# Kernel tuning notes

Measured on AMD Instinct MI355X. Metric: run time of the kernel, lower is better.

## Reference

```python
import jax, jax.numpy as jnp
import numpy as np

N_NODES = 50000
N_EDGES = 640000
HID = 128
EDGE_FEAT = 4
NUM_G = 20
R_MIN, R_MAX = 0.0, 10.0

def setup_inputs() -> dict:
    key = jax.random.key(0)
    ks = jax.random.split(key, 16)
    s = lambda d: 1.0 / np.sqrt(d)
    return {
        'h': jax.random.normal(ks[0], (N_NODES, HID), jnp.float32),
        'x': jax.random.normal(ks[1], (N_NODES, 3), jnp.float32),
        'edge_index': jax.random.randint(ks[2], (2, N_EDGES), 0, N_NODES, dtype=jnp.int64),
        'mask_ligand': jnp.ones((N_NODES,), jnp.float32),
        'edge_attr': jax.random.normal(ks[3], (N_EDGES, EDGE_FEAT), jnp.float32),
        'We1': jax.random.normal(ks[4], (2*HID+EDGE_FEAT+NUM_G, HID), jnp.float32) * s(2*HID+EDGE_FEAT+NUM_G),
        'be1': jnp.zeros((HID,), jnp.float32),
        'We2': jax.random.normal(ks[5], (HID, HID), jnp.float32) * s(HID),
        'be2': jnp.zeros((HID,), jnp.float32),
        'Winf': jax.random.normal(ks[6], (HID, 1), jnp.float32) * s(HID),
        'binf': jnp.zeros((1,), jnp.float32),
        'Wx1': jax.random.normal(ks[7], (HID, HID), jnp.float32) * s(HID),
        'bx1': jnp.zeros((HID,), jnp.float32),
        'Wx2': jax.random.normal(ks[8], (HID, 1), jnp.float32) * 0.001 * s(HID),
        'Wn1': jax.random.normal(ks[9], (2*HID, HID), jnp.float32) * s(2*HID),
        'bn1': jnp.zeros((HID,), jnp.float32),
        'Wn2': jax.random.normal(ks[10], (HID, HID), jnp.float32) * s(HID),
        'bn2': jnp.zeros((HID,), jnp.float32),
    }

def reference(h, x, edge_index, mask_ligand, edge_attr,
              We1, be1, We2, be2, Winf, binf, Wx1, bx1, Wx2, Wn1, bn1, Wn2, bn2):
    n = h.shape[0]
    src, dst = edge_index[0], edge_index[1]
    hi, hj = h[dst], h[src]                      # [E, H] gathers
    rel_x = x[dst] - x[src]                      # [E, 3]
    d_sq = jnp.sum(rel_x**2, axis=-1, keepdims=True)  # [E, 1]
    d = jnp.sqrt(d_sq + 1e-8)
    # GaussianSmearing(r_min=0, r_max=10, num_gaussians=20)
    offset = jnp.linspace(R_MIN, R_MAX, NUM_G, dtype=h.dtype)
    coeff = -0.5 / (offset[1] - offset[0])**2
    d_feat = jnp.exp(coeff * (d - offset)**2)    # [E, 20]
    edge_feat = jnp.concatenate([d_feat, edge_attr], axis=-1)
    # edge MLP (2 layers, silu, act_last=True)
    z = jnp.concatenate([hi, hj, edge_feat], axis=-1)
    mij = jax.nn.silu(jax.nn.silu(z @ We1 + be1) @ We2 + be2)  # [E, H]
    eij = jax.nn.sigmoid(mij @ Winf + binf)      # [E, 1]
    mi = jax.ops.segment_sum(mij * eij, dst, num_segments=n)   # [N, H]
    # node MLP (2 layers, silu, no act on last)
    nz = jnp.concatenate([mi, h], axis=-1)
    h_out = h + (jax.nn.silu(nz @ Wn1 + bn1) @ Wn2 + bn2)
    # coordinate update
    xg = jnp.tanh(jax.nn.silu(mij @ Wx1 + bx1) @ Wx2)          # [E, 1]
    delta_x = jax.ops.segment_sum(rel_x / (d + 1.0) * xg, dst, num_segments=n)
    x_out = x + delta_x * mask_ligand[:, None]
    return h_out, x_out
```

## Files before the change

kernel.cpp:

```cpp
#include <hip/hip_runtime.h>
#include <math.h>

#define NN 50000
#define NE 640000
#define H 128
#define EPB 32
#define NPB 32
#define ZB 296
#define BB 136
#define KP1 288
#define NZB 264

typedef __attribute__((ext_vector_type(8))) unsigned short u16x8;
typedef __attribute__((ext_vector_type(8))) __bf16 bf16x8;
typedef __attribute__((ext_vector_type(2))) __bf16 bf16x2;
typedef __attribute__((ext_vector_type(4))) float f32x4;

__device__ __forceinline__ float silu_f(float v) {
    return v / (1.0f + __expf(-v));
}

__device__ __forceinline__ unsigned short f2bf(float f) {
    unsigned int u = __builtin_bit_cast(unsigned int, f);
    u += 0x7FFFu + ((u >> 16) & 1u);
    return (unsigned short)(u >> 16);
}

__device__ __forceinline__ float bf2f(unsigned short s) {
    unsigned int u = ((unsigned int)s) << 16;
    return __builtin_bit_cast(float, u);
}

__device__ __forceinline__ unsigned int pkbf(float lo, float hi) {
#if __has_builtin(__builtin_amdgcn_cvt_pk_bf16_f32)
    bf16x2 v = __builtin_amdgcn_cvt_pk_bf16_f32(lo, hi);
    unsigned int r; __builtin_memcpy(&r, &v, 4); return r;
#else
    return (unsigned int)f2bf(lo) | ((unsigned int)f2bf(hi) << 16);
#endif
}

__device__ __forceinline__ f32x4 mfma16(u16x8 a, u16x8 b, f32x4 c) {
    return __builtin_amdgcn_mfma_f32_16x16x32_bf16(
        __builtin_bit_cast(bf16x8, a), __builtin_bit_cast(bf16x8, b), c, 0, 0, 0);
}

template<int KT, int INSTR, bool SYNC_BEFORE_EPI>
__device__ __forceinline__ void layer_mfma(
    const unsigned short* __restrict__ inbuf,
    const unsigned short* __restrict__ wt,
    const float* __restrict__ bias,
    unsigned short* __restrict__ outbuf,
    int wv, int quad, int r16)
{
    f32x4 acc[2][2] = {};
    const int F = wv * 32;
    #pragma unroll
    for (int ks = 0; ks < KT / 32; ks++) {
        int ko = ks * 32 + quad * 8;
        u16x8 b0 = *(const u16x8*)(inbuf + r16 * INSTR + ko);
        u16x8 b1 = *(const u16x8*)(inbuf + (16 + r16) * INSTR + ko);
        u16x8 a0 = *(const u16x8*)(wt + (size_t)(F + r16) * KT + ko);
        u16x8 a1 = *(const u16x8*)(wt + (size_t)(F + 16 + r16) * KT + ko);
        acc[0][0] = mfma16(a0, b0, acc[0][0]);
        acc[0][1] = mfma16(a0, b1, acc[0][1]);
        acc[1][0] = mfma16(a1, b0, acc[1][0]);
        acc[1][1] = mfma16(a1, b1, acc[1][1]);
    }
    if (SYNC_BEFORE_EPI) __syncthreads();
    #pragma unroll
    for (int rt = 0; rt < 2; rt++) {
        int f0 = F + rt * 16 + quad * 4;
        float4 bv = *(const float4*)(bias + f0);
        #pragma unroll
        for (int ci = 0; ci < 2; ci++) {
            int e = ci * 16 + r16;
            float s0 = silu_f(acc[rt][ci][0] + bv.x);
            float s1 = silu_f(acc[rt][ci][1] + bv.y);
            float s2 = silu_f(acc[rt][ci][2] + bv.z);
            float s3 = silu_f(acc[rt][ci][3] + bv.w);
            uint2 p = { pkbf(s0, s1), pkbf(s2, s3) };
            *(uint2*)(outbuf + e * BB + f0) = p;
        }
    }
}

__global__ __launch_bounds__(256) void convert_weights(
    const float* __restrict__ We1, const float* __restrict__ We2,
    const float* __restrict__ Wx1, const float* __restrict__ Wn1,
    const float* __restrict__ Wn2,
    unsigned short* __restrict__ w1t, unsigned short* __restrict__ w2t,
    unsigned short* __restrict__ wx1t, unsigned short* __restrict__ wn1t,
    unsigned short* __restrict__ wn2t)
{
    int i = blockIdx.x * 256 + threadIdx.x;
    const int S1 = 128 * KP1;
    const int S2 = 128 * 128;
    const int S3 = 128 * 256;
    if (i < S1) {
        int n = i / KP1, k = i % KP1;
        w1t[i] = (k < 280) ? f2bf(We1[k * H + n]) : (unsigned short)0;
    } else if (i < S1 + S2) {
        int j = i - S1; int n = j / H, k = j % H;
        w2t[j] = f2bf(We2[k * H + n]);
    } else if (i < S1 + 2 * S2) {
        int j = i - S1 - S2; int n = j / H, k = j % H;
        wx1t[j] = f2bf(Wx1[k * H + n]);
    } else if (i < S1 + 2 * S2 + S3) {
        int j = i - S1 - 2 * S2; int n = j / 256, k = j % 256;
        wn1t[j] = f2bf(Wn1[k * H + n]);
    } else if (i < S1 + 3 * S2 + S3) {
        int j = i - S1 - 2 * S2 - S3; int n = j / H, k = j % H;
        wn2t[j] = f2bf(Wn2[k * H + n]);
    }
}

__global__ __launch_bounds__(256) void zero_kernel(float4* __restrict__ p, int n4) {
    int i = blockIdx.x * 256 + threadIdx.x;
    if (i < n4) p[i] = make_float4(0.f, 0.f, 0.f, 0.f);
}

__global__ __launch_bounds__(256, 5) void edge_kernel(
    const float* __restrict__ h, const float* __restrict__ x,
    const int* __restrict__ ei, const float* __restrict__ edge_attr,
    const unsigned short* __restrict__ w1t, const float* __restrict__ be1,
    const unsigned short* __restrict__ w2t, const float* __restrict__ be2,
    const float* __restrict__ Winf, const float* __restrict__ binf,
    const unsigned short* __restrict__ wx1t, const float* __restrict__ bx1,
    const float* __restrict__ Wx2,
    float* __restrict__ mi, float* __restrict__ dx)
{
    __shared__ unsigned short zs[EPB * ZB];
    __shared__ unsigned short m2[EPB * BB];
    __shared__ float relx_s[EPB][3];
    __shared__ float eij_s[EPB];
    __shared__ float xg_s[EPB];
    __shared__ int dst_s[EPB];
    __shared__ int src_s[EPB];
    __shared__ float winf_s[H];
    __shared__ float wx2_s[H];

    unsigned short* m1 = zs;

    const int t = threadIdx.x;
    const int e0 = blockIdx.x * EPB;

    if (t < EPB) {
        src_s[t] = ei[e0 + t];
        dst_s[t] = ei[NE + e0 + t];
    }
    if (t >= 128 && t < 256) {
        winf_s[t - 128] = Winf[t - 128];
        wx2_s[t - 128] = Wx2[t - 128];
    }
    __syncthreads();

    {
        int e = t >> 3, l = t & 7;
        int s = src_s[e], d = dst_s[e];
        const float4* hd = (const float4*)(h + (size_t)d * H);
        const float4* hs = (const float4*)(h + (size_t)s * H);
        unsigned short* zr = zs + e * ZB;
        float4 v0 = hd[l * 4 + 0], v1 = hd[l * 4 + 1];
        float4 v2 = hd[l * 4 + 2], v3 = hd[l * 4 + 3];
        uint4 p0 = { pkbf(v0.x, v0.y), pkbf(v0.z, v0.w), pkbf(v1.x, v1.y), pkbf(v1.z, v1.w) };
        uint4 p1 = { pkbf(v2.x, v2.y), pkbf(v2.z, v2.w), pkbf(v3.x, v3.y), pkbf(v3.z, v3.w) };
        *(uint4*)(zr + l * 16) = p0;
        *(uint4*)(zr + l * 16 + 8) = p1;
        float4 w0 = hs[l * 4 + 0], w1 = hs[l * 4 + 1];
        float4 w2 = hs[l * 4 + 2], w3 = hs[l * 4 + 3];
        uint4 q0 = { pkbf(w0.x, w0.y), pkbf(w0.z, w0.w), pkbf(w1.x, w1.y), pkbf(w1.z, w1.w) };
        uint4 q1 = { pkbf(w2.x, w2.y), pkbf(w2.z, w2.w), pkbf(w3.x, w3.y), pkbf(w3.z, w3.w) };
        *(uint4*)(zr + 128 + l * 16) = q0;
        *(uint4*)(zr + 128 + l * 16 + 8) = q1;
    }
    if (t < EPB) {
        int s = src_s[t], d = dst_s[t];
        float rx = x[d * 3 + 0] - x[s * 3 + 0];
        float ry = x[d * 3 + 1] - x[s * 3 + 1];
        float rz = x[d * 3 + 2] - x[s * 3 + 2];
        float d2 = rx * rx + ry * ry + rz * rz;
        float dd = sqrtf(d2 + 1e-8f);
        float inv = 1.0f / (dd + 1.0f);
        relx_s[t][0] = rx * inv;
        relx_s[t][1] = ry * inv;
        relx_s[t][2] = rz * inv;
        const float step = 10.0f / 19.0f;
        const float coeff = -0.5f / (step * step);
        unsigned short* zr = zs + t * ZB;
        #pragma unroll
        for (int g = 0; g < 20; g++) {
            float df = dd - step * (float)g;
            zr[256 + g] = f2bf(__expf(coeff * df * df));
        }
        #pragma unroll
        for (int j = 0; j < 4; j++)
            zr[276 + j] = f2bf(edge_attr[(size_t)(e0 + t) * 4 + j]);
        #pragma unroll
        for (int j = 280; j < ZB; j++) zr[j] = 0;
    }
    __syncthreads();

    const int wv = t >> 6, lane = t & 63;
    const int quad = lane >> 4, r16 = lane & 15;

    layer_mfma<KP1, ZB, true>(zs, w1t, be1, m1, wv, quad, r16);
    __syncthreads();

    layer_mfma<H, BB, false>(m1, w2t, be2, m2, wv, quad, r16);
    __syncthreads();

    {
        int e = t >> 3, l = t & 7;
        const unsigned short* row = m2 + e * BB + l * 16;
        u16x8 v0 = *(const u16x8*)(row);
        u16x8 v1 = *(const u16x8*)(row + 8);
        float s = 0.0f;
        #pragma unroll
        for (int j = 0; j < 8; j++) {
            s += bf2f(v0[j]) * winf_s[l * 16 + j];
            s += bf2f(v1[j]) * winf_s[l * 16 + 8 + j];
        }
        s += __shfl_down(s, 4, 8);
        s += __shfl_down(s, 2, 8);
        s += __shfl_down(s, 1, 8);
        if (l == 0) eij_s[e] = 1.0f / (1.0f + __expf(-(s + binf[0])));
    }

    layer_mfma<H, BB, false>(m2, wx1t, bx1, m1, wv, quad, r16);
    __syncthreads();

    {
        int e = t >> 3, l = t & 7;
        const unsigned short* row = m1 + e * BB + l * 16;
        u16x8 v0 = *(const u16x8*)(row);
        u16x8 v1 = *(const u16x8*)(row + 8);
        float s = 0.0f;
        #pragma unroll
        for (int j = 0; j < 8; j++) {
            s += bf2f(v0[j]) * wx2_s[l * 16 + j];
            s += bf2f(v1[j]) * wx2_s[l * 16 + 8 + j];
        }
        s += __shfl_down(s, 4, 8);
        s += __shfl_down(s, 2, 8);
        s += __shfl_down(s, 1, 8);
        if (l == 0) xg_s[e] = tanhf(s);
    }
    __syncthreads();

    {
        int k = t & 127, eh = t >> 7;
        for (int e = eh; e < EPB; e += 2) {
            float mv = bf2f(m2[e * BB + k]) * eij_s[e];
            atomicAdd(&mi[(size_t)dst_s[e] * H + k], mv);
        }
        if (t < EPB * 3) {
            int e = t / 3, dim = t % 3;
            atomicAdd(&dx[(size_t)dst_s[e] * 3 + dim], relx_s[e][dim] * xg_s[e]);
        }
    }
}

__global__ __launch_bounds__(256, 6) void node_kernel(
    const float* __restrict__ h, const float* __restrict__ x,
    const float* __restrict__ mask,
    const unsigned short* __restrict__ wn1t, const float* __restrict__ bn1,
    const unsigned short* __restrict__ wn2t, const float* __restrict__ bn2,
    float* __restrict__ mi_hout, float* __restrict__ dx_xout)
{
    __shared__ unsigned short nzs[NPB * NZB];
    __shared__ unsigned short nbuf[NPB * BB];

    const int t = threadIdx.x;
    const int n0 = blockIdx.x * NPB;

    {
        int r = t >> 3, l = t & 7;
        int n = n0 + r;
        unsigned short* zr = nzs + r * NZB;
        if (n < NN) {
            const float4* mi4 = (const float4*)(mi_hout + (size_t)n * H);
            const float4* h4  = (const float4*)(h + (size_t)n * H);
            float4 v0 = mi4[l * 4 + 0], v1 = mi4[l * 4 + 1];
            float4 v2 = mi4[l * 4 + 2], v3 = mi4[l * 4 + 3];
            uint4 p0 = { pkbf(v0.x, v0.y), pkbf(v0.z, v0.w), pkbf(v1.x, v1.y), pkbf(v1.z, v1.w) };
            uint4 p1 = { pkbf(v2.x, v2.y), pkbf(v2.z, v2.w), pkbf(v3.x, v3.y), pkbf(v3.z, v3.w) };
            *(uint4*)(zr + l * 16) = p0;
            *(uint4*)(zr + l * 16 + 8) = p1;
            float4 w0 = h4[l * 4 + 0], w1 = h4[l * 4 + 1];
            float4 w2 = h4[l * 4 + 2], w3 = h4[l * 4 + 3];
            uint4 q0 = { pkbf(w0.x, w0.y), pkbf(w0.z, w0.w), pkbf(w1.x, w1.y), pkbf(w1.z, w1.w) };
            uint4 q1 = { pkbf(w2.x, w2.y), pkbf(w2.z, w2.w), pkbf(w3.x, w3.y), pkbf(w3.z, w3.w) };
            *(uint4*)(zr + 128 + l * 16) = q0;
            *(uint4*)(zr + 128 + l * 16 + 8) = q1;
        } else {
            uint4 zf = {0u, 0u, 0u, 0u};
            *(uint4*)(zr + l * 16) = zf;
            *(uint4*)(zr + l * 16 + 8) = zf;
            *(uint4*)(zr + 128 + l * 16) = zf;
            *(uint4*)(zr + 128 + l * 16 + 8) = zf;
        }
    }

    float xo = 0.f;
    int xn = -1, xdim = 0;
    if (t < NPB * 3) {
        int r = t / 3; xdim = t % 3;
        int n = n0 + r;
        if (n < NN) {
            xn = n;
            xo = x[(size_t)n * 3 + xdim] + dx_xout[(size_t)n * 3 + xdim] * mask[n];
        }
    }
    __syncthreads();

    if (xn >= 0) dx_xout[(size_t)xn * 3 + xdim] = xo;

    const int wv = t >> 6, lane = t & 63;
    const int quad = lane >> 4, r16 = lane & 15;

    layer_mfma<2 * H, NZB, false>(nzs, wn1t, bn1, nbuf, wv, quad, r16);
    __syncthreads();

    {
        f32x4 acc[2][2] = {};
        const int F = wv * 32;
        #pragma unroll
        for (int ks = 0; ks < H / 32; ks++) {
            int ko = ks * 32 + quad * 8;
            u16x8 b0 = *(const u16x8*)(nbuf + r16 * BB + ko);
            u16x8 b1 = *(const u16x8*)(nbuf + (16 + r16) * BB + ko);
            u16x8 a0 = *(const u16x8*)(wn2t + (size_t)(F + r16) * H + ko);
            u16x8 a1 = *(const u16x8*)(wn2t + (size_t)(F + 16 + r16) * H + ko);
            acc[0][0] = mfma16(a0, b0, acc[0][0]);
            acc[0][1] = mfma16(a0, b1, acc[0][1]);
            acc[1][0] = mfma16(a1, b0, acc[1][0]);
            acc[1][1] = mfma16(a1, b1, acc[1][1]);
        }
        #pragma unroll
        for (int rt = 0; rt < 2; rt++) {
            int f0 = F + rt * 16 + quad * 4;
            float4 bv = *(const float4*)(bn2 + f0);
            #pragma unroll
            for (int ci = 0; ci < 2; ci++) {
                int n = n0 + ci * 16 + r16;
                if (n < NN) {
                    float4 hv = *(const float4*)(h + (size_t)n * H + f0);
                    float4 o;
                    o.x = hv.x + acc[rt][ci][0] + bv.x;
                    o.y = hv.y + acc[rt][ci][1] + bv.y;
                    o.z = hv.z + acc[rt][ci][2] + bv.z;
                    o.w = hv.w + acc[rt][ci][3] + bv.w;
                    *(float4*)(mi_hout + (size_t)n * H + f0) = o;
                }
            }
        }
    }
}

extern "C" void kernel_launch(void* const* d_in, const int* in_sizes, int n_in,
                              void* d_out, int out_size, void* d_ws, size_t ws_size,
                              hipStream_t stream) {
    const float* h     = (const float*)d_in[0];
    const float* x     = (const float*)d_in[1];
    const int*   ei    = (const int*)d_in[2];
    const float* mask  = (const float*)d_in[3];
    const float* eattr = (const float*)d_in[4];
    const float* We1   = (const float*)d_in[5];
    const float* be1   = (const float*)d_in[6];
    const float* We2   = (const float*)d_in[7];
    const float* be2   = (const float*)d_in[8];
    const float* Winf  = (const float*)d_in[9];
    const float* binf  = (const float*)d_in[10];
    const float* Wx1   = (const float*)d_in[11];
    const float* bx1   = (const float*)d_in[12];
    const float* Wx2   = (const float*)d_in[13];
    const float* Wn1   = (const float*)d_in[14];
    const float* bn1   = (const float*)d_in[15];
    const float* Wn2   = (const float*)d_in[16];
    const float* bn2   = (const float*)d_in[17];

    float* mi = (float*)d_out;
    float* dx = mi + (size_t)NN * H;

    unsigned short* w1t  = (unsigned short*)d_ws;
    unsigned short* w2t  = w1t + 128 * KP1;
    unsigned short* wx1t = w2t + 128 * H;
    unsigned short* wn1t = wx1t + 128 * H;
    unsigned short* wn2t = wn1t + 128 * 256;

    const int wconv_total = 128 * KP1 + 3 * 128 * H + 128 * 256;
    convert_weights<<<(wconv_total + 255) / 256, 256, 0, stream>>>(
        We1, We2, Wx1, Wn1, Wn2, w1t, w2t, wx1t, wn1t, wn2t);

    const int total4 = (NN * H + NN * 3) / 4;
    zero_kernel<<<(total4 + 255) / 256, 256, 0, stream>>>((float4*)d_out, total4);

    edge_kernel<<<NE / EPB, 256, 0, stream>>>(
        h, x, ei, eattr, w1t, be1, w2t, be2, Winf, binf, wx1t, bx1, Wx2, mi, dx);

    node_kernel<<<(NN + NPB - 1) / NPB, 256, 0, stream>>>(
        h, x, mask, wn1t, bn1, wn2t, bn2, mi, dx);
}
```

Baseline: 525.0 us.

## Fuse edge-gate and coord-gate dot products into MFMA epilogues, scatter from registers

Layers 2 and 3 of the edge kernel are inlined. The Winf and Wx2 dot products are computed in the MFMA epilogue from registers, reduced with cross-lane shuffles and then through small shared per-wave partial arrays. This removes the separate shared-memory reread passes and the xg/eij reduction passes. The mi scatter now uses fp32 silu values held in registers instead of the bf16 copy in shared memory. The cost is more live registers, so the launch-bounds occupancy hint drops from 5 to 4 blocks per CU, and the atomics use a less coalesced pattern of 4 consecutive floats per lane.

```diff
diff --git a/kernel.cpp b/kernel.cpp
--- a/kernel.cpp
+++ b/kernel.cpp
@@ -120,7 +120,7 @@
     if (i < n4) p[i] = make_float4(0.f, 0.f, 0.f, 0.f);
 }
 
-__global__ __launch_bounds__(256, 5) void edge_kernel(
+__global__ __launch_bounds__(256, 4) void edge_kernel(
     const float* __restrict__ h, const float* __restrict__ x,
     const int* __restrict__ ei, const float* __restrict__ edge_attr,
     const unsigned short* __restrict__ w1t, const float* __restrict__ be1,
@@ -134,7 +134,8 @@
     __shared__ unsigned short m2[EPB * BB];
     __shared__ float relx_s[EPB][3];
     __shared__ float eij_s[EPB];
-    __shared__ float xg_s[EPB];
+    __shared__ float epart[4][EPB];
+    __shared__ float xpart[4][EPB];
     __shared__ int dst_s[EPB];
     __shared__ int src_s[EPB];
     __shared__ float winf_s[H];
@@ -203,61 +204,123 @@
 
     const int wv = t >> 6, lane = t & 63;
     const int quad = lane >> 4, r16 = lane & 15;
+    const int F = wv * 32;
 
     layer_mfma<KP1, ZB, true>(zs, w1t, be1, m1, wv, quad, r16);
     __syncthreads();
 
-    layer_mfma<H, BB, false>(m1, w2t, be2, m2, wv, quad, r16);
-    __syncthreads();
-
+    float sil[2][2][4];
     {
-        int e = t >> 3, l = t & 7;
-        const unsigned short* row = m2 + e * BB + l * 16;
-        u16x8 v0 = *(const u16x8*)(row);
-        u16x8 v1 = *(const u16x8*)(row + 8);
-        float s = 0.0f;
-        #pragma unroll
-        for (int j = 0; j < 8; j++) {
-            s += bf2f(v0[j]) * winf_s[l * 16 + j];
-            s += bf2f(v1[j]) * winf_s[l * 16 + 8 + j];
-        }
-        s += __shfl_down(s, 4, 8);
-        s += __shfl_down(s, 2, 8);
-        s += __shfl_down(s, 1, 8);
-        if (l == 0) eij_s[e] = 1.0f / (1.0f + __expf(-(s + binf[0])));
-    }
-
-    layer_mfma<H, BB, false>(m2, wx1t, bx1, m1, wv, quad, r16);
-    __syncthreads();
+        f32x4 acc[2][2] = {};
+        #pragma unroll
+        for (int ks = 0; ks < H / 32; ks++) {
+            int ko = ks * 32 + quad * 8;
+            u16x8 b0 = *(const u16x8*)(m1 + r16 * BB + ko);
+            u16x8 b1 = *(const u16x8*)(m1 + (16 + r16) * BB + ko);
+            u16x8 a0 = *(const u16x8*)(w2t + (size_t)(F + r16) * H + ko);
+            u16x8 a1 = *(const u16x8*)(w2t + (size_t)(F + 16 + r16) * H + ko);
+            acc[0][0] = mfma16(a0, b0, acc[0][0]);
+            acc[0][1] = mfma16(a0, b1, acc[0][1]);
+            acc[1][0] = mfma16(a1, b0, acc[1][0]);
+            acc[1][1] = mfma16(a1, b1, acc[1][1]);
+        }
+        float ep[2] = {0.f, 0.f};
+        #pragma unroll
+        for (int rt = 0; rt < 2; rt++) {
+            int f0 = F + rt * 16 + quad * 4;
+            float4 bv = *(const float4*)(be2 + f0);
+            float4 wf = *(const float4*)(winf_s + f0);
+            #pragma unroll
+            for (int ci = 0; ci < 2; ci++) {
+                int e = ci * 16 + r16;
+                float s0 = silu_f(acc[rt][ci][0] + bv.x);
+                float s1 = silu_f(acc[rt][ci][1] + bv.y);
+                float s2 = silu_f(acc[rt][ci][2] + bv.z);
+                float s3 = silu_f(acc[rt][ci][3] + bv.w);
+                sil[rt][ci][0] = s0; sil[rt][ci][1] = s1;
+                sil[rt][ci][2] = s2; sil[rt][ci][3] = s3;
+                ep[ci] += s0 * wf.x + s1 * wf.y + s2 * wf.z + s3 * wf.w;
+                uint2 p = { pkbf(s0, s1), pkbf(s2, s3) };
+                *(uint2*)(m2 + e * BB + f0) = p;
+            }
+        }
+        #pragma unroll
+        for (int ci = 0; ci < 2; ci++) {
+            ep[ci] += __shfl_xor(ep[ci], 16, 64);
+            ep[ci] += __shfl_xor(ep[ci], 32, 64);
+        }
+        if (quad == 0) {
+            epart[wv][r16] = ep[0];
+            epart[wv][16 + r16] = ep[1];
+        }
+    }
+    __syncthreads();
+
+    if (t < EPB) {
+        float s = epart[0][t] + epart[1][t] + epart[2][t] + epart[3][t] + binf[0];
+        eij_s[t] = 1.0f / (1.0f + __expf(-s));
+    }
 
     {
-        int e = t >> 3, l = t & 7;
-        const unsigned short* row = m1 + e * BB + l * 16;
-        u16x8 v0 = *(const u16x8*)(row);
-        u16x8 v1 = *(const u16x8*)(row + 8);
-        float s = 0.0f;
-        #pragma unroll
-        for (int j = 0; j < 8; j++) {
-            s += bf2f(v0[j]) * wx2_s[l * 16 + j];
-            s += bf2f(v1[j]) * wx2_s[l * 16 + 8 + j];
-        }
-        s += __shfl_down(s, 4, 8);
-        s += __shfl_down(s, 2, 8);
-        s += __shfl_down(s, 1, 8);
-        if (l == 0) xg_s[e] = tanhf(s);
-    }
-    __syncthreads();
-
-    {
-        int k = t & 127, eh = t >> 7;
-        for (int e = eh; e < EPB; e += 2) {
-            float mv = bf2f(m2[e * BB + k]) * eij_s[e];
-            atomicAdd(&mi[(size_t)dst_s[e] * H + k], mv);
-        }
-        if (t < EPB * 3) {
-            int e = t / 3, dim = t % 3;
-            atomicAdd(&dx[(size_t)dst_s[e] * 3 + dim], relx_s[e][dim] * xg_s[e]);
-        }
+        f32x4 acc[2][2] = {};
+        #pragma unroll
+        for (int ks = 0; ks < H / 32; ks++) {
+            int ko = ks * 32 + quad * 8;
+            u16x8 b0 = *(const u16x8*)(m2 + r16 * BB + ko);
+            u16x8 b1 = *(const u16x8*)(m2 + (16 + r16) * BB + ko);
+            u16x8 a0 = *(const u16x8*)(wx1t + (size_t)(F + r16) * H + ko);
+            u16x8 a1 = *(const u16x8*)(wx1t + (size_t)(F + 16 + r16) * H + ko);
+            acc[0][0] = mfma16(a0, b0, acc[0][0]);
+            acc[0][1] = mfma16(a0, b1, acc[0][1]);
+            acc[1][0] = mfma16(a1, b0, acc[1][0]);
+            acc[1][1] = mfma16(a1, b1, acc[1][1]);
+        }
+        float xp[2] = {0.f, 0.f};
+        #pragma unroll
+        for (int rt = 0; rt < 2; rt++) {
+            int f0 = F + rt * 16 + quad * 4;
+            float4 bv = *(const float4*)(bx1 + f0);
+            float4 wf = *(const float4*)(wx2_s + f0);
+            #pragma unroll
+            for (int ci = 0; ci < 2; ci++) {
+                xp[ci] += silu_f(acc[rt][ci][0] + bv.x) * wf.x
+                        + silu_f(acc[rt][ci][1] + bv.y) * wf.y
+                        + silu_f(acc[rt][ci][2] + bv.z) * wf.z
+                        + silu_f(acc[rt][ci][3] + bv.w) * wf.w;
+            }
+        }
+        #pragma unroll
+        for (int ci = 0; ci < 2; ci++) {
+            xp[ci] += __shfl_xor(xp[ci], 16, 64);
+            xp[ci] += __shfl_xor(xp[ci], 32, 64);
+        }
+        if (quad == 0) {
+            xpart[wv][r16] = xp[0];
+            xpart[wv][16 + r16] = xp[1];
+        }
+    }
+    __syncthreads();
+
+    #pragma unroll
+    for (int ci = 0; ci < 2; ci++) {
+        int e = ci * 16 + r16;
+        float eij = eij_s[e];
+        float* row = mi + (size_t)dst_s[e] * H;
+        #pragma unroll
+        for (int rt = 0; rt < 2; rt++) {
+            int f0 = F + rt * 16 + quad * 4;
+            atomicAdd(row + f0 + 0, sil[rt][ci][0] * eij);
+            atomicAdd(row + f0 + 1, sil[rt][ci][1] * eij);
+            atomicAdd(row + f0 + 2, sil[rt][ci][2] * eij);
+            atomicAdd(row + f0 + 3, sil[rt][ci][3] * eij);
+        }
+    }
+
+    if (t < EPB * 3) {
+        int e = t / 3, dim = t % 3;
+        float xs = xpart[0][e] + xpart[1][e] + xpart[2][e] + xpart[3][e];
+        float xg = tanhf(xs);
+        atomicAdd(&dx[(size_t)dst_s[e] * 3 + dim], relx_s[e][dim] * xg);
     }
 }
 
```

Measured after the change: 1.284 ms. +144.5%, slower.
